# Optimization experiments

Measured on AMD Instinct MI355X. Metric: run time of the kernel, lower is better.

## Reference

```python
import jax, jax.numpy as jnp
import numpy as np

DT = 0.1  # leak rate of the FORCE rate-RNN cell


def setup_inputs() -> dict:
    key = jax.random.key(0)
    ks = jax.random.split(key, 6)
    N, IN, OUT, T = 192, 64, 192, 32
    alpha_P = 1.0
    x = jax.random.normal(ks[0], (1, T, IN), jnp.float32)
    y = jax.random.normal(ks[1], (1, T, OUT), jnp.float32)
    W_in = jax.random.normal(ks[2], (IN, N), jnp.float32) / np.sqrt(IN).astype(np.float32)
    W_rec = 1.5 * jax.random.normal(ks[3], (N, N), jnp.float32) / np.sqrt(N).astype(np.float32)
    W_out = jax.random.normal(ks[4], (N, OUT), jnp.float32) / np.sqrt(N).astype(np.float32)
    a0 = jax.random.normal(ks[5], (1, N), jnp.float32)
    # P_output = alpha_P * I  (keras.initializers.Identity(gain=alpha_P))
    P_output = alpha_P * jnp.eye(N, dtype=jnp.float32)
    # P_GG: identity_3d[:, i, i] = alpha_P -> each of the N slices is alpha_P * I
    P_GG = jnp.broadcast_to(alpha_P * jnp.eye(N, dtype=jnp.float32), (N, N, N)).copy()
    return dict(x=x, y=y, W_in=W_in, W_rec=W_rec, W_out=W_out, a0=a0,
                P_output=P_output, P_GG=P_GG)


def _step(carry, xy, W_in):
    a, P_o, W_o, P_g, W_r = carry
    x_t, y_t = xy  # (IN,), (N,)
    # leaky tanh rate-RNN cell (canonical tension FORCE layer)
    a = (1.0 - DT) * a + DT * (jnp.tanh(a) @ W_r + x_t[None, :] @ W_in)  # (1,N)
    h = jnp.tanh(a)[0]            # (N,)
    z = h @ W_o                   # (N,)
    # --- RLS / Sherman-Morrison update of P_output ---
    k = P_o @ h                   # (N,)
    c = 1.0 / (1.0 + h @ k)
    P_o = P_o - c * jnp.outer(k, h @ P_o)
    # --- output kernel update (uses UPDATED P_output, SGD lr=1) ---
    e = z - y_t                   # (N,)
    W_o = W_o - jnp.outer(P_o @ h, e)
    # --- per-neuron RLS update of P_GG (N,N,N) ---
    Ph = jnp.einsum('ijk,k->ij', P_g, h)      # (N,N)
    hPh = Ph @ h                              # (N,)
    htP = jnp.einsum('k,ikj->ij', h, P_g)     # (N,N)
    P_g = P_g - Ph[:, :, None] * htP[:, None, :] / (1.0 + hPh)[:, None, None]
    # --- recurrent kernel update (uses UPDATED P_GG) ---
    Ph2 = jnp.einsum('ijk,k->ij', P_g, h)     # (N,N)
    W_r = W_r - (Ph2 * e[None, :]).T
    return (a, P_o, W_o, P_g, W_r), z


def reference(x, y, W_in, W_rec, W_out, a0, P_output, P_GG):
    def step(carry, xy):
        return _step(carry, xy, W_in)
    carry0 = (a0, P_output, W_out, P_GG, W_rec)
    _, zs = jax.lax.scan(step, carry0, (x[0], y[0]))  # zs: (T, N)
    return zs[None, :, :]  # (1, T, N): readout sequence during FORCE training
```

## Files before the change

kernel.cpp:

```cpp
#include <hip/hip_runtime.h>
#include <math.h>

#define NN   192
#define NIN  64
#define NT   32
#define BLK  192
#define NW   3

typedef unsigned long long u64;

struct WS {
  u64 hslot[NN];
  u64 ekslot[NN][2];
};

#define REP48(M) M(0)M(1)M(2)M(3)M(4)M(5)M(6)M(7)M(8)M(9)M(10)M(11)M(12)M(13)M(14)M(15)M(16)M(17)M(18)M(19)M(20)M(21)M(22)M(23)M(24)M(25)M(26)M(27)M(28)M(29)M(30)M(31)M(32)M(33)M(34)M(35)M(36)M(37)M(38)M(39)M(40)M(41)M(42)M(43)M(44)M(45)M(46)M(47)

__device__ __forceinline__ u64 packf(float v, unsigned tag) {
  return ((u64)tag << 32) | (u64)__float_as_uint(v);
}

__device__ __forceinline__ float poll_slot(u64* p, unsigned tag) {
  u64 v; long g = 0;
  while (true) {
    v = __hip_atomic_load(p, __ATOMIC_RELAXED, __HIP_MEMORY_SCOPE_AGENT);
    if ((unsigned)(v >> 32) == tag) break;
    __builtin_amdgcn_s_sleep(1);
    if (++g > 30000000L) break;
  }
  return __uint_as_float((unsigned)v);
}

__device__ __forceinline__ float2 poll_ek(u64* p, unsigned tag) {
  u64 va, vb; long g = 0;
  while (true) {
    va = __hip_atomic_load(p,     __ATOMIC_RELAXED, __HIP_MEMORY_SCOPE_AGENT);
    vb = __hip_atomic_load(p + 1, __ATOMIC_RELAXED, __HIP_MEMORY_SCOPE_AGENT);
    if (((unsigned)(va >> 32) == tag) & ((unsigned)(vb >> 32) == tag)) break;
    __builtin_amdgcn_s_sleep(1);
    if (++g > 30000000L) break;
  }
  return make_float2(__uint_as_float((unsigned)va), __uint_as_float((unsigned)vb));
}

template <int K>
__device__ __forceinline__ void block_reduceK(float* v, float (*red)[NW], int w, int l) {
  #pragma unroll
  for (int o = 32; o > 0; o >>= 1) {
    #pragma unroll
    for (int q = 0; q < K; ++q) v[q] += __shfl_xor(v[q], o, 64);
  }
  if (l == 0) {
    #pragma unroll
    for (int q = 0; q < K; ++q) red[q][w] = v[q];
  }
  __syncthreads();
  #pragma unroll
  for (int q = 0; q < K; ++q) v[q] = red[q][0] + red[q][1] + red[q][2];
}

extern "C" __global__ void __launch_bounds__(BLK, 1)
force_persistent(const float* __restrict__ x,   const float* __restrict__ y,
                 const float* __restrict__ Win, const float* __restrict__ Wrec,
                 const float* __restrict__ Wout,const float* __restrict__ a0,
                 const float* __restrict__ Pout,const float* __restrict__ Pgg,
                 float* __restrict__ out, WS* __restrict__ ws)
{
  const int b   = blockIdx.x;
  const int tid = threadIdx.x;
  const int w   = tid >> 6;
  const int l   = tid & 63;

  __shared__ __align__(16) float hsS[NN];
  __shared__ __align__(16) float phS[NN];
  __shared__ float red5[2][5][NW];
  __shared__ float red3[2][3][NW];
  __shared__ float xwS[NT];
  __shared__ float yS [NT];

  if (w == 0) {
    const float wv = Win[l * NN + b];
    float c[NT];
    #pragma unroll
    for (int t2 = 0; t2 < NT; ++t2) c[t2] = x[t2 * NIN + l] * wv;
    #pragma unroll
    for (int o = 32; o > 0; o >>= 1) {
      #pragma unroll
      for (int t2 = 0; t2 < NT; ++t2) c[t2] += __shfl_xor(c[t2], o, 64);
    }
    if (l == 0) {
      #pragma unroll
      for (int t2 = 0; t2 < NT; ++t2) xwS[t2] = c[t2];
    }
  } else if (w == 1 && l < NT) {
    yS[l] = y[l * NN + b];
  }

  float wrt = Wrec[tid * NN + b];
  float wot = Wout[tid * NN + b];
  float po  = Pout[b * NN + tid];

  float a_run;
  {
    float v0[1] = { tanhf(a0[tid]) * wrt };
    block_reduceK<1>(v0, red3[1], w, l);
    a_run = 0.9f * a0[b] + 0.1f * (v0[0] + xwS[0]);
    if (tid == 0)
      __hip_atomic_store(&ws->hslot[b], packf(tanhf(a_run), 1u),
                         __ATOMIC_RELAXED, __HIP_MEMORY_SCOPE_AGENT);
  }

  #define SDECL(r) float4 s##r;
  REP48(SDECL)
  {
    const float4* srow = (const float4*)(Pgg + (size_t)b * NN * NN + (size_t)tid * NN);
    #define SLOAD(r) s##r = srow[r];
    REP48(SLOAD)
  }

  float p_prev = 0.f, rden_prev = 0.f, c_prev = 0.f;
  float e_prev_own = 0.f, k_prev_own = 0.f, e_b_prev = 0.f, k_b_prev = 0.f;

  #pragma unroll 1
  for (int t = 0; t < NT; ++t) {
    const unsigned tag = (unsigned)(t + 1);
    const int par = t & 1;

    const float h_own = poll_slot(&ws->hslot[tid], tag);
    hsS[tid] = h_own;

    float v[5];
    v[0] = h_own * wrt;
    v[1] = h_own * (p_prev * e_prev_own);
    v[2] = h_own * wot;
    v[3] = h_own * k_prev_own;
    v[4] = h_own * po;
    block_reduceK<5>(v, red5[par], w, l);
    const float ssum_half = v[0] - rden_prev * v[1];
    const float g   = v[3];
    const float z   = v[2] - c_prev * e_b_prev * g;
    const float kb  = v[4] - c_prev * k_b_prev * g;
    const float eb  = z - yS[t];
    if (tid == 0) {
      __hip_atomic_store(&ws->ekslot[b][0], packf(eb, tag),
                         __ATOMIC_RELAXED, __HIP_MEMORY_SCOPE_AGENT);
      __hip_atomic_store(&ws->ekslot[b][1], packf(kb, tag),
                         __ATOMIC_RELAXED, __HIP_MEMORY_SCOPE_AGENT);
      out[t * NN + b] = z;
    }
    if (t == NT - 1) break;

    wrt -= rden_prev * p_prev * e_prev_own;
    wot -= c_prev * k_prev_own * e_b_prev;
    po  -= c_prev * k_b_prev  * k_prev_own;

    const float4* h4 = (const float4*)hsS;
    float4 acc = make_float4(0.f, 0.f, 0.f, 0.f);
    #define PHC(r) { const float4 hv = h4[r]; \
                     acc.x += s##r.x*hv.x; acc.y += s##r.y*hv.y; \
                     acc.z += s##r.z*hv.z; acc.w += s##r.w*hv.w; }
    REP48(PHC)
    const float p = (acc.x + acc.y) + (acc.z + acc.w);
    phS[tid] = p;

    const float2 ek = poll_ek(&ws->ekslot[tid][0], tag);
    const float e_own = ek.x, k_own = ek.y;

    float u[3];
    u[0] = k_own * h_own;
    u[1] = h_own * p * e_own;
    u[2] = p * h_own;
    block_reduceK<3>(u, red3[par], w, l);
    const float rden = 1.f / (1.f + u[2]);
    const float c1   = 1.f / (1.f + u[0]);

    a_run = 0.9f * a_run + 0.1f * (ssum_half - rden * u[1] + xwS[t + 1]);
    if (tid == 0)
      __hip_atomic_store(&ws->hslot[b], packf(tanhf(a_run), tag + 1u),
                         __ATOMIC_RELAXED, __HIP_MEMORY_SCOPE_AGENT);

    const float rv = rden * p;
    const float4* ph4 = (const float4*)phS;
    #define PHD(r) { const float4 pv = ph4[r]; \
                     s##r.x -= rv*pv.x; s##r.y -= rv*pv.y; \
                     s##r.z -= rv*pv.z; s##r.w -= rv*pv.w; }
    REP48(PHD)

    p_prev = p; rden_prev = rden; c_prev = c1;
    e_prev_own = e_own; k_prev_own = k_own; e_b_prev = eb; k_b_prev = kb;
  }
}

extern "C" void kernel_launch(void* const* d_in, const int* in_sizes, int n_in,
                              void* d_out, int out_size, void* d_ws, size_t ws_size,
                              hipStream_t stream) {
  const float* x    = (const float*)d_in[0];
  const float* y    = (const float*)d_in[1];
  const float* Win  = (const float*)d_in[2];
  const float* Wrec = (const float*)d_in[3];
  const float* Wout = (const float*)d_in[4];
  const float* a0   = (const float*)d_in[5];
  const float* Pout = (const float*)d_in[6];
  const float* Pgg  = (const float*)d_in[7];
  float* out = (float*)d_out;
  WS* ws = (WS*)d_ws;
  (void)in_sizes; (void)n_in; (void)out_size; (void)ws_size;

  hipMemsetAsync(ws, 0, sizeof(WS), stream);
  force_persistent<<<NN, BLK, 0, stream>>>(x, y, Win, Wrec, Wout, a0, Pout, Pgg, out, ws);
}
```

Before: 139.2 us.

## Replicate per-consumer broadcast slots and pack step tags into mantissa bits

Each block now writes its h value, and its e/k pair, into a separate slot for every consumer block, using one thread per consumer. Each consumer therefore polls its own contiguous row instead of all blocks hammering the same shared slots. The step tag is folded into the low 8 mantissa bits, so e and k fit in a single 64-bit atomic and h fits in 32 bits, halving the polled words. In exchange, values lose 8 mantissa bits, the workspace becomes much larger (and so does the memset that clears it), and each step performs many more scattered global stores.

After: 151.5 us. 1.09x slower.

```diff
diff --git a/kernel.cpp b/kernel.cpp
--- a/kernel.cpp
+++ b/kernel.cpp
@@ -8,39 +8,44 @@
 #define NW   3
 
 typedef unsigned long long u64;
+typedef unsigned int u32;
 
 struct WS {
-  u64 hslot[NN];
-  u64 ekslot[NN][2];
+  u32 hrep [NN][NN];
+  u64 ekrep[NN][NN];
 };
 
 #define REP48(M) M(0)M(1)M(2)M(3)M(4)M(5)M(6)M(7)M(8)M(9)M(10)M(11)M(12)M(13)M(14)M(15)M(16)M(17)M(18)M(19)M(20)M(21)M(22)M(23)M(24)M(25)M(26)M(27)M(28)M(29)M(30)M(31)M(32)M(33)M(34)M(35)M(36)M(37)M(38)M(39)M(40)M(41)M(42)M(43)M(44)M(45)M(46)M(47)
 
-__device__ __forceinline__ u64 packf(float v, unsigned tag) {
-  return ((u64)tag << 32) | (u64)__float_as_uint(v);
-}
-
-__device__ __forceinline__ float poll_slot(u64* p, unsigned tag) {
+__device__ __forceinline__ u32 pack_h(float v, u32 tag) {
+  return (__float_as_uint(v) & ~0xFFu) | tag;
+}
+__device__ __forceinline__ u64 pack_ek(float e, float k, u32 tag) {
+  return ((u64)((__float_as_uint(e) & ~0xFFu) | tag) << 32)
+       |  (u64)((__float_as_uint(k) & ~0xFFu) | tag);
+}
+
+__device__ __forceinline__ float poll_h(u32* p, u32 tag) {
+  u32 v; long g = 0;
+  while (true) {
+    v = __hip_atomic_load(p, __ATOMIC_RELAXED, __HIP_MEMORY_SCOPE_AGENT);
+    if ((v & 0xFFu) == tag) break;
+    __builtin_amdgcn_s_sleep(1);
+    if (++g > 30000000L) break;
+  }
+  return __uint_as_float(v & ~0xFFu);
+}
+
+__device__ __forceinline__ float2 poll_ek(u64* p, u32 tag) {
   u64 v; long g = 0;
   while (true) {
     v = __hip_atomic_load(p, __ATOMIC_RELAXED, __HIP_MEMORY_SCOPE_AGENT);
-    if ((unsigned)(v >> 32) == tag) break;
+    if ((((u32)v & 0xFFu) == tag) & (((u32)(v >> 32) & 0xFFu) == tag)) break;
     __builtin_amdgcn_s_sleep(1);
     if (++g > 30000000L) break;
   }
-  return __uint_as_float((unsigned)v);
-}
-
-__device__ __forceinline__ float2 poll_ek(u64* p, unsigned tag) {
-  u64 va, vb; long g = 0;
-  while (true) {
-    va = __hip_atomic_load(p,     __ATOMIC_RELAXED, __HIP_MEMORY_SCOPE_AGENT);
-    vb = __hip_atomic_load(p + 1, __ATOMIC_RELAXED, __HIP_MEMORY_SCOPE_AGENT);
-    if (((unsigned)(va >> 32) == tag) & ((unsigned)(vb >> 32) == tag)) break;
-    __builtin_amdgcn_s_sleep(1);
-    if (++g > 30000000L) break;
-  }
-  return make_float2(__uint_as_float((unsigned)va), __uint_as_float((unsigned)vb));
+  return make_float2(__uint_as_float((u32)(v >> 32) & ~0xFFu),
+                     __uint_as_float((u32)v & ~0xFFu));
 }
 
 template <int K>
@@ -105,9 +110,8 @@
     float v0[1] = { tanhf(a0[tid]) * wrt };
     block_reduceK<1>(v0, red3[1], w, l);
     a_run = 0.9f * a0[b] + 0.1f * (v0[0] + xwS[0]);
-    if (tid == 0)
-      __hip_atomic_store(&ws->hslot[b], packf(tanhf(a_run), 1u),
-                         __ATOMIC_RELAXED, __HIP_MEMORY_SCOPE_AGENT);
+    __hip_atomic_store(&ws->hrep[tid][b], pack_h(tanhf(a_run), 1u),
+                       __ATOMIC_RELAXED, __HIP_MEMORY_SCOPE_AGENT);
   }
 
   #define SDECL(r) float4 s##r;
@@ -123,10 +127,10 @@
 
   #pragma unroll 1
   for (int t = 0; t < NT; ++t) {
-    const unsigned tag = (unsigned)(t + 1);
+    const u32 tag = (u32)(t + 1);
     const int par = t & 1;
 
-    const float h_own = poll_slot(&ws->hslot[tid], tag);
+    const float h_own = poll_h(&ws->hrep[b][tid], tag);
     hsS[tid] = h_own;
 
     float v[5];
@@ -141,13 +145,9 @@
     const float z   = v[2] - c_prev * e_b_prev * g;
     const float kb  = v[4] - c_prev * k_b_prev * g;
     const float eb  = z - yS[t];
-    if (tid == 0) {
-      __hip_atomic_store(&ws->ekslot[b][0], packf(eb, tag),
-                         __ATOMIC_RELAXED, __HIP_MEMORY_SCOPE_AGENT);
-      __hip_atomic_store(&ws->ekslot[b][1], packf(kb, tag),
-                         __ATOMIC_RELAXED, __HIP_MEMORY_SCOPE_AGENT);
-      out[t * NN + b] = z;
-    }
+    __hip_atomic_store(&ws->ekrep[tid][b], pack_ek(eb, kb, tag),
+                       __ATOMIC_RELAXED, __HIP_MEMORY_SCOPE_AGENT);
+    if (tid == 0) out[t * NN + b] = z;
     if (t == NT - 1) break;
 
     wrt -= rden_prev * p_prev * e_prev_own;
@@ -163,7 +163,7 @@
     const float p = (acc.x + acc.y) + (acc.z + acc.w);
     phS[tid] = p;
 
-    const float2 ek = poll_ek(&ws->ekslot[tid][0], tag);
+    const float2 ek = poll_ek(&ws->ekrep[b][tid], tag);
     const float e_own = ek.x, k_own = ek.y;
 
     float u[3];
@@ -175,9 +175,9 @@
     const float c1   = 1.f / (1.f + u[0]);
 
     a_run = 0.9f * a_run + 0.1f * (ssum_half - rden * u[1] + xwS[t + 1]);
-    if (tid == 0)
-      __hip_atomic_store(&ws->hslot[b], packf(tanhf(a_run), tag + 1u),
-                         __ATOMIC_RELAXED, __HIP_MEMORY_SCOPE_AGENT);
+    const float hnext = tanhf(a_run);
+    __hip_atomic_store(&ws->hrep[tid][b], pack_h(hnext, tag + 1u),
+                       __ATOMIC_RELAXED, __HIP_MEMORY_SCOPE_AGENT);
 
     const float rv = rden * p;
     const float4* ph4 = (const float4*)phS;
```

## Add per-step arrival counters so one thread waits before block polls slots

Applied to the files above, without the earlier changes.

Adds global per-timestep arrival counters. Thread 0 of each block spins on the counter and then releases the rest of the block through a shared-memory hint, so 192 threads no longer each poll remote tagged slots. It also splits the block reduction so the rden term is reduced before waiting on e/k, overlapping that work with the wait, and replaces tanhf with a fast exp/rcp approximation. The cost is extra atomics per step and a two-level spin, plus small precision loss from the fast tanh.

Result: slower. 226.8 us (+63.0%).

```diff
diff --git a/kernel.cpp b/kernel.cpp
--- a/kernel.cpp
+++ b/kernel.cpp
@@ -8,39 +8,64 @@
 #define NW   3
 
 typedef unsigned long long u64;
+typedef unsigned int u32;
 
 struct WS {
   u64 hslot[NN];
   u64 ekslot[NN][2];
+  int hcnt [NT][16];
+  int ekcnt[NT][16];
 };
 
 #define REP48(M) M(0)M(1)M(2)M(3)M(4)M(5)M(6)M(7)M(8)M(9)M(10)M(11)M(12)M(13)M(14)M(15)M(16)M(17)M(18)M(19)M(20)M(21)M(22)M(23)M(24)M(25)M(26)M(27)M(28)M(29)M(30)M(31)M(32)M(33)M(34)M(35)M(36)M(37)M(38)M(39)M(40)M(41)M(42)M(43)M(44)M(45)M(46)M(47)
 
-__device__ __forceinline__ u64 packf(float v, unsigned tag) {
+__device__ __forceinline__ u64 packf(float v, u32 tag) {
   return ((u64)tag << 32) | (u64)__float_as_uint(v);
 }
 
-__device__ __forceinline__ float poll_slot(u64* p, unsigned tag) {
+__device__ __forceinline__ float tanh_fast(float x) {
+  x = fminf(fmaxf(x, -15.f), 15.f);
+  const float e = __expf(-2.f * x);
+  return (1.f - e) * __builtin_amdgcn_rcpf(1.f + e);
+}
+
+__device__ __forceinline__ float poll_slot(u64* p, u32 tag) {
   u64 v; long g = 0;
   while (true) {
     v = __hip_atomic_load(p, __ATOMIC_RELAXED, __HIP_MEMORY_SCOPE_AGENT);
-    if ((unsigned)(v >> 32) == tag) break;
+    if ((u32)(v >> 32) == tag) break;
     __builtin_amdgcn_s_sleep(1);
     if (++g > 30000000L) break;
   }
-  return __uint_as_float((unsigned)v);
-}
-
-__device__ __forceinline__ float2 poll_ek(u64* p, unsigned tag) {
+  return __uint_as_float((u32)v);
+}
+
+__device__ __forceinline__ float2 poll_ek(u64* p, u32 tag) {
   u64 va, vb; long g = 0;
   while (true) {
     va = __hip_atomic_load(p,     __ATOMIC_RELAXED, __HIP_MEMORY_SCOPE_AGENT);
     vb = __hip_atomic_load(p + 1, __ATOMIC_RELAXED, __HIP_MEMORY_SCOPE_AGENT);
-    if (((unsigned)(va >> 32) == tag) & ((unsigned)(vb >> 32) == tag)) break;
+    if (((u32)(va >> 32) == tag) & ((u32)(vb >> 32) == tag)) break;
     __builtin_amdgcn_s_sleep(1);
     if (++g > 30000000L) break;
   }
-  return make_float2(__uint_as_float((unsigned)va), __uint_as_float((unsigned)vb));
+  return make_float2(__uint_as_float((u32)va), __uint_as_float((u32)vb));
+}
+
+__device__ __forceinline__ void hint_wait(int* cnt, int* hintS, int want, int tid) {
+  if (tid == 0) {
+    long g = 0;
+    while (__hip_atomic_load(cnt, __ATOMIC_RELAXED, __HIP_MEMORY_SCOPE_AGENT) < NN) {
+      __builtin_amdgcn_s_sleep(1);
+      if (++g > 30000000L) break;
+    }
+    __hip_atomic_store(hintS, want, __ATOMIC_RELAXED, __HIP_MEMORY_SCOPE_WORKGROUP);
+  }
+  long g = 0;
+  while (__hip_atomic_load(hintS, __ATOMIC_RELAXED, __HIP_MEMORY_SCOPE_WORKGROUP) < want) {
+    __builtin_amdgcn_s_sleep(1);
+    if (++g > 100000000L) break;
+  }
 }
 
 template <int K>
@@ -74,9 +99,13 @@
   __shared__ __align__(16) float hsS[NN];
   __shared__ __align__(16) float phS[NN];
   __shared__ float red5[2][5][NW];
-  __shared__ float red3[2][3][NW];
+  __shared__ float red1[2][1][NW];
+  __shared__ float red2[2][2][NW];
   __shared__ float xwS[NT];
   __shared__ float yS [NT];
+  __shared__ int   hintS;
+
+  if (tid == 0) hintS = 0;
 
   if (w == 0) {
     const float wv = Win[l * NN + b];
@@ -102,12 +131,15 @@
 
   float a_run;
   {
-    float v0[1] = { tanhf(a0[tid]) * wrt };
-    block_reduceK<1>(v0, red3[1], w, l);
+    float v0[1] = { tanh_fast(a0[tid]) * wrt };
+    block_reduceK<1>(v0, red1[1], w, l);
     a_run = 0.9f * a0[b] + 0.1f * (v0[0] + xwS[0]);
-    if (tid == 0)
-      __hip_atomic_store(&ws->hslot[b], packf(tanhf(a_run), 1u),
-                         __ATOMIC_RELAXED, __HIP_MEMORY_SCOPE_AGENT);
+    if (tid == 0) {
+      __hip_atomic_store(&ws->hslot[b], packf(tanh_fast(a_run), 1u),
+                         __ATOMIC_RELAXED, __HIP_MEMORY_SCOPE_AGENT);
+      __hip_atomic_fetch_add(&ws->hcnt[0][0], 1,
+                             __ATOMIC_RELAXED, __HIP_MEMORY_SCOPE_AGENT);
+    }
   }
 
   #define SDECL(r) float4 s##r;
@@ -123,9 +155,10 @@
 
   #pragma unroll 1
   for (int t = 0; t < NT; ++t) {
-    const unsigned tag = (unsigned)(t + 1);
+    const u32 tag = (u32)(t + 1);
     const int par = t & 1;
 
+    hint_wait(&ws->hcnt[t][0], &hintS, 2 * t + 1, tid);
     const float h_own = poll_slot(&ws->hslot[tid], tag);
     hsS[tid] = h_own;
 
@@ -146,6 +179,8 @@
                          __ATOMIC_RELAXED, __HIP_MEMORY_SCOPE_AGENT);
       __hip_atomic_store(&ws->ekslot[b][1], packf(kb, tag),
                          __ATOMIC_RELAXED, __HIP_MEMORY_SCOPE_AGENT);
+      __hip_atomic_fetch_add(&ws->ekcnt[t][0], 1,
+                             __ATOMIC_RELAXED, __HIP_MEMORY_SCOPE_AGENT);
       out[t * NN + b] = z;
     }
     if (t == NT - 1) break;
@@ -162,24 +197,30 @@
     REP48(PHC)
     const float p = (acc.x + acc.y) + (acc.z + acc.w);
     phS[tid] = p;
-
+    const float hp = h_own * p;
+
+    float u1[1] = { hp };
+    block_reduceK<1>(u1, red1[par], w, l);
+    const float rden = 1.f / (1.f + u1[0]);
+    const float rv   = rden * p;
+
+    hint_wait(&ws->ekcnt[t][0], &hintS, 2 * t + 2, tid);
     const float2 ek = poll_ek(&ws->ekslot[tid][0], tag);
     const float e_own = ek.x, k_own = ek.y;
 
-    float u[3];
+    float u[2];
     u[0] = k_own * h_own;
-    u[1] = h_own * p * e_own;
-    u[2] = p * h_own;
-    block_reduceK<3>(u, red3[par], w, l);
-    const float rden = 1.f / (1.f + u[2]);
-    const float c1   = 1.f / (1.f + u[0]);
-
+    u[1] = hp * e_own;
+    block_reduceK<2>(u, red2[par], w, l);
     a_run = 0.9f * a_run + 0.1f * (ssum_half - rden * u[1] + xwS[t + 1]);
-    if (tid == 0)
-      __hip_atomic_store(&ws->hslot[b], packf(tanhf(a_run), tag + 1u),
-                         __ATOMIC_RELAXED, __HIP_MEMORY_SCOPE_AGENT);
-
-    const float rv = rden * p;
+    if (tid == 0) {
+      __hip_atomic_store(&ws->hslot[b], packf(tanh_fast(a_run), tag + 1u),
+                         __ATOMIC_RELAXED, __HIP_MEMORY_SCOPE_AGENT);
+      __hip_atomic_fetch_add(&ws->hcnt[t + 1][0], 1,
+                             __ATOMIC_RELAXED, __HIP_MEMORY_SCOPE_AGENT);
+    }
+    const float c1 = 1.f / (1.f + u[0]);
+
     const float4* ph4 = (const float4*)phS;
     #define PHD(r) { const float4 pv = ph4[r]; \
                      s##r.x -= rv*pv.x; s##r.y -= rv*pv.y; \
```
